# Performance work log

Measured on AMD Instinct MI355X. Metric: run time of the kernel, lower is better.

Reference implementation:

```python
import jax, jax.numpy as jnp
import numpy as np
import math

DEC = (4, 4, 4)  # (vertical=Y, horizontal=X, depth=Z)


def _idct_mat(N, dtype=jnp.float32):
    # orthonormal DCT-II matrix D[k,n]; IDCT (DCT-III ortho) is D.T
    k = jnp.arange(N, dtype=dtype)[:, None]
    n = jnp.arange(N, dtype=dtype)[None, :]
    D = jnp.cos(jnp.pi * (n + 0.5) * k / N)
    s = jnp.where(k == 0, jnp.sqrt(1.0 / N), jnp.sqrt(2.0 / N))
    return (s * D).T  # [n, k]: y[n] = sum_k IDCT[n,k] X[k]


def _permute_idct_coefs(x, dec):
    decY, decX, decZ = dec
    coefs = x.reshape(-1, decY * decX * decZ)
    chY, chX, chZ = (decY + 1) // 2, (decX + 1) // 2, (decZ + 1) // 2
    fhY, fhX, fhZ = decY // 2, decX // 2, decZ // 2
    sizes = [(chY, chX, chZ), (chY, chX, fhZ), (chY, fhX, chZ), (chY, fhX, fhZ),
             (fhY, chX, chZ), (fhY, chX, fhZ), (fhY, fhX, chZ), (fhY, fhX, fhZ)]
    nB = coefs.shape[0]
    value = jnp.zeros((nB, decY, decX, decZ), dtype=x.dtype)
    slices = [(slice(0, None, 2), slice(0, None, 2), slice(0, None, 2)),
              (slice(0, None, 2), slice(0, None, 2), slice(1, None, 2)),
              (slice(0, None, 2), slice(1, None, 2), slice(0, None, 2)),
              (slice(0, None, 2), slice(1, None, 2), slice(1, None, 2)),
              (slice(1, None, 2), slice(0, None, 2), slice(0, None, 2)),
              (slice(1, None, 2), slice(0, None, 2), slice(1, None, 2)),
              (slice(1, None, 2), slice(1, None, 2), slice(0, None, 2)),
              (slice(1, None, 2), slice(1, None, 2), slice(1, None, 2))]
    start = 0
    for (sy, sx, sz), (ny, nx, nz) in zip(slices, sizes):
        n = ny * nx * nz
        chunk = coefs[:, start:start + n].reshape(nB, ny, nx, nz)
        value = value.at[:, sy, sx, sz].set(chunk)
        start += n
    return value


def setup_inputs() -> dict:
    key = jax.random.key(0)
    x0 = jax.random.normal(key, (4, 64, 64, 64, DEC[0] * DEC[1] * DEC[2]), dtype=jnp.float32)
    return {"x0": x0}


def reference(x0) -> jnp.ndarray:
    nsamples, nrows, ncols, nlays, _ = x0.shape
    decY, decX, decZ = DEC
    V = _permute_idct_coefs(x0, DEC)  # [nBlocks, decY, decX, decZ]
    IY, IX, IZ = _idct_mat(decY, x0.dtype), _idct_mat(decX, x0.dtype), _idct_mat(decZ, x0.dtype)
    # separable 3D IDCT (orthonormal) along the three block axes
    Y = jnp.einsum('byxz,iy,jx,kz->bijk', V, IY, IX, IZ)
    height, width, depth = nrows * decY, ncols * decX, nlays * decZ
    Z = Y.reshape(nsamples, 1, height, width, depth)
    return Z
```

## Files before the change

kernel.cpp:

```cpp
#include <hip/hip_runtime.h>


#define WG 128
#define ROWS 68

__device__ __constant__ float Mc[4][4] = {
    { 0.5f,  0.6532814824381883f,  0.5f,  0.2705980500730985f },
    { 0.5f,  0.2705980500730985f, -0.5f, -0.6532814824381883f },
    { 0.5f, -0.2705980500730985f, -0.5f,  0.6532814824381883f },
    { 0.5f, -0.6532814824381883f,  0.5f, -0.2705980500730985f },
};

__global__ __launch_bounds__(WG) void nsolt_idct3d_kernel(
    const float* __restrict__ in, float* __restrict__ out)
{
    __shared__ float lds[WG * ROWS];
    const int t = threadIdx.x;
    const size_t base = (size_t)blockIdx.x * (WG * 64);

#pragma unroll
    for (int m = 0; m < 16; ++m) {
        const int e = m * (WG * 4) + t * 4;
        const float4 q = *reinterpret_cast<const float4*>(in + base + e);
        const int row = e >> 6;
        const int col = e & 63;
        *reinterpret_cast<float4*>(&lds[row * ROWS + col]) = q;
    }
    __syncthreads();

    float* __restrict__ myrow = &lds[t * ROWS];

    float M[4][4];
#pragma unroll
    for (int a = 0; a < 4; ++a)
#pragma unroll
        for (int b = 0; b < 4; ++b) M[a][b] = Mc[a][b];

    float A[64];
#pragma unroll
    for (int y = 0; y < 4; ++y) {
#pragma unroll
        for (int x = 0; x < 4; ++x) {
            float vz[4];
#pragma unroll
            for (int z = 0; z < 4; ++z) {
                const int chunk  = (y & 1) * 4 + (x & 1) * 2 + (z & 1);
                const int within = (y >> 1) * 4 + (x >> 1) * 2 + (z >> 1);
                vz[z] = myrow[chunk * 8 + within];
            }
#pragma unroll
            for (int k = 0; k < 4; ++k) {
                A[(y * 4 + x) * 4 + k] =
                    M[k][0] * vz[0] + M[k][1] * vz[1] +
                    M[k][2] * vz[2] + M[k][3] * vz[3];
            }
        }
    }

#pragma unroll
    for (int y = 0; y < 4; ++y) {
        float tmp[16];
#pragma unroll
        for (int j = 0; j < 4; ++j)
#pragma unroll
            for (int k = 0; k < 4; ++k)
                tmp[j * 4 + k] =
                    M[j][0] * A[y * 16 + 0 * 4 + k] +
                    M[j][1] * A[y * 16 + 1 * 4 + k] +
                    M[j][2] * A[y * 16 + 2 * 4 + k] +
                    M[j][3] * A[y * 16 + 3 * 4 + k];
#pragma unroll
        for (int n = 0; n < 16; ++n) A[y * 16 + n] = tmp[n];
    }

#pragma unroll
    for (int i = 0; i < 4; ++i) {
#pragma unroll
        for (int j = 0; j < 4; ++j) {
            float r0 = M[i][0] * A[0 * 16 + j * 4 + 0] + M[i][1] * A[1 * 16 + j * 4 + 0] +
                       M[i][2] * A[2 * 16 + j * 4 + 0] + M[i][3] * A[3 * 16 + j * 4 + 0];
            float r1 = M[i][0] * A[0 * 16 + j * 4 + 1] + M[i][1] * A[1 * 16 + j * 4 + 1] +
                       M[i][2] * A[2 * 16 + j * 4 + 1] + M[i][3] * A[3 * 16 + j * 4 + 1];
            float r2 = M[i][0] * A[0 * 16 + j * 4 + 2] + M[i][1] * A[1 * 16 + j * 4 + 2] +
                       M[i][2] * A[2 * 16 + j * 4 + 2] + M[i][3] * A[3 * 16 + j * 4 + 2];
            float r3 = M[i][0] * A[0 * 16 + j * 4 + 3] + M[i][1] * A[1 * 16 + j * 4 + 3] +
                       M[i][2] * A[2 * 16 + j * 4 + 3] + M[i][3] * A[3 * 16 + j * 4 + 3];
            float4 q;
            q.x = r0; q.y = r1; q.z = r2; q.w = r3;
            *reinterpret_cast<float4*>(&myrow[i * 16 + j * 4]) = q;
        }
    }
    __syncthreads();

#pragma unroll
    for (int m = 0; m < 16; ++m) {
        const int e = m * (WG * 4) + t * 4;
        const int row = e >> 6;
        const int col = e & 63;
        const float4 q = *reinterpret_cast<const float4*>(&lds[row * ROWS + col]);
        *reinterpret_cast<float4*>(out + base + e) = q;
    }
}

extern "C" void kernel_launch(void* const* d_in, const int* in_sizes, int n_in,
                              void* d_out, int out_size, void* d_ws, size_t ws_size,
                              hipStream_t stream)
{
    const float* in = (const float*)d_in[0];
    float* out = (float*)d_out;

    const long long nBlocks = (long long)in_sizes[0] / 64;
    const int grid = (int)(nBlocks / WG);

    hipLaunchKernelGGL(nsolt_idct3d_kernel, dim3(grid), dim3(WG), 0, stream,
                       in, out);
}
```

Before: 103.7 us.

## Use butterfly 4-point IDCT, vectorized LDS gathers, and smaller workgroup

Replaces the dense 4x4 matrix products in each of the three separable IDCT passes with an even/odd butterfly factorization, cutting multiply-adds per point. The coefficient gather from LDS now uses float4 reads instead of scalar reads. The workgroup size drops from 128 to 64, which doubles the grid and lowers LDS per block. The final pass now writes to LDS with scalar stores instead of float4 stores, which may add LDS store traffic.

New measurement: 100.1 us. 1.04x faster.

```diff
diff --git a/kernel.cpp b/kernel.cpp
--- a/kernel.cpp
+++ b/kernel.cpp
@@ -1,15 +1,23 @@
 #include <hip/hip_runtime.h>
 
 
-#define WG 128
+#define WG 64
 #define ROWS 68
 
-__device__ __constant__ float Mc[4][4] = {
-    { 0.5f,  0.6532814824381883f,  0.5f,  0.2705980500730985f },
-    { 0.5f,  0.2705980500730985f, -0.5f, -0.6532814824381883f },
-    { 0.5f, -0.2705980500730985f, -0.5f,  0.6532814824381883f },
-    { 0.5f, -0.6532814824381883f,  0.5f, -0.2705980500730985f },
-};
+#define C1F 0.6532814824381883f
+#define C3F 0.2705980500730985f
+
+#define IDCT4(a0, a2, a1, a3, r0, r1, r2, r3)            \
+    {                                                    \
+        const float e0 = 0.5f * ((a0) + (a2));           \
+        const float e1 = 0.5f * ((a0) - (a2));           \
+        const float o0 = C1F * (a1) + C3F * (a3);        \
+        const float o1 = C3F * (a1) - C1F * (a3);        \
+        (r0) = e0 + o0;                                  \
+        (r1) = e1 + o1;                                  \
+        (r2) = e1 - o1;                                  \
+        (r3) = e0 - o0;                                  \
+    }
 
 __global__ __launch_bounds__(WG) void nsolt_idct3d_kernel(
     const float* __restrict__ in, float* __restrict__ out)
@@ -30,64 +38,45 @@
 
     float* __restrict__ myrow = &lds[t * ROWS];
 
-    float M[4][4];
+    float A[4][4][4];
 #pragma unroll
-    for (int a = 0; a < 4; ++a)
+    for (int c2 = 0; c2 < 2; ++c2) {
 #pragma unroll
-        for (int b = 0; b < 4; ++b) M[a][b] = Mc[a][b];
-
-    float A[64];
+        for (int w2 = 0; w2 < 2; ++w2) {
+            const int y = 2 * w2 + c2;
 #pragma unroll
-    for (int y = 0; y < 4; ++y) {
-#pragma unroll
-        for (int x = 0; x < 4; ++x) {
-            float vz[4];
-#pragma unroll
-            for (int z = 0; z < 4; ++z) {
-                const int chunk  = (y & 1) * 4 + (x & 1) * 2 + (z & 1);
-                const int within = (y >> 1) * 4 + (x >> 1) * 2 + (z >> 1);
-                vz[z] = myrow[chunk * 8 + within];
-            }
-#pragma unroll
-            for (int k = 0; k < 4; ++k) {
-                A[(y * 4 + x) * 4 + k] =
-                    M[k][0] * vz[0] + M[k][1] * vz[1] +
-                    M[k][2] * vz[2] + M[k][3] * vz[3];
+            for (int c1 = 0; c1 < 2; ++c1) {
+                const int b0 = c2 * 32 + c1 * 16 + w2 * 4;
+                const float4 q0 = *reinterpret_cast<const float4*>(&myrow[b0]);
+                const float4 q1 = *reinterpret_cast<const float4*>(&myrow[b0 + 8]);
+                IDCT4(q0.x, q0.y, q1.x, q1.y,
+                      A[y][c1][0], A[y][c1][1], A[y][c1][2], A[y][c1][3]);
+                IDCT4(q0.z, q0.w, q1.z, q1.w,
+                      A[y][2 + c1][0], A[y][2 + c1][1], A[y][2 + c1][2], A[y][2 + c1][3]);
             }
         }
     }
 
+    float B[4][4][4];
 #pragma unroll
     for (int y = 0; y < 4; ++y) {
-        float tmp[16];
 #pragma unroll
-        for (int j = 0; j < 4; ++j)
-#pragma unroll
-            for (int k = 0; k < 4; ++k)
-                tmp[j * 4 + k] =
-                    M[j][0] * A[y * 16 + 0 * 4 + k] +
-                    M[j][1] * A[y * 16 + 1 * 4 + k] +
-                    M[j][2] * A[y * 16 + 2 * 4 + k] +
-                    M[j][3] * A[y * 16 + 3 * 4 + k];
-#pragma unroll
-        for (int n = 0; n < 16; ++n) A[y * 16 + n] = tmp[n];
+        for (int n = 0; n < 4; ++n) {
+            IDCT4(A[y][0][n], A[y][2][n], A[y][1][n], A[y][3][n],
+                  B[y][0][n], B[y][1][n], B[y][2][n], B[y][3][n]);
+        }
     }
 
 #pragma unroll
-    for (int i = 0; i < 4; ++i) {
+    for (int j = 0; j < 4; ++j) {
 #pragma unroll
-        for (int j = 0; j < 4; ++j) {
-            float r0 = M[i][0] * A[0 * 16 + j * 4 + 0] + M[i][1] * A[1 * 16 + j * 4 + 0] +
-                       M[i][2] * A[2 * 16 + j * 4 + 0] + M[i][3] * A[3 * 16 + j * 4 + 0];
-            float r1 = M[i][0] * A[0 * 16 + j * 4 + 1] + M[i][1] * A[1 * 16 + j * 4 + 1] +
-                       M[i][2] * A[2 * 16 + j * 4 + 1] + M[i][3] * A[3 * 16 + j * 4 + 1];
-            float r2 = M[i][0] * A[0 * 16 + j * 4 + 2] + M[i][1] * A[1 * 16 + j * 4 + 2] +
-                       M[i][2] * A[2 * 16 + j * 4 + 2] + M[i][3] * A[3 * 16 + j * 4 + 2];
-            float r3 = M[i][0] * A[0 * 16 + j * 4 + 3] + M[i][1] * A[1 * 16 + j * 4 + 3] +
-                       M[i][2] * A[2 * 16 + j * 4 + 3] + M[i][3] * A[3 * 16 + j * 4 + 3];
-            float4 q;
-            q.x = r0; q.y = r1; q.z = r2; q.w = r3;
-            *reinterpret_cast<float4*>(&myrow[i * 16 + j * 4]) = q;
+        for (int n = 0; n < 4; ++n) {
+            float r0, r1, r2, r3;
+            IDCT4(B[0][j][n], B[2][j][n], B[1][j][n], B[3][j][n], r0, r1, r2, r3);
+            myrow[0 * 16 + j * 4 + n] = r0;
+            myrow[1 * 16 + j * 4 + n] = r1;
+            myrow[2 * 16 + j * 4 + n] = r2;
+            myrow[3 * 16 + j * 4 + n] = r3;
         }
     }
     __syncthreads();
```
